# Kernel tuning notes

Hardware: AMD Instinct MI355X
Metric: run time of the kernel (lower is better)

## Reference

```python
import jax, jax.numpy as jnp
import numpy as np

D_MODEL = 1024
NUM_HEADS = 16
D_K = D_MODEL // NUM_HEADS
ROPE_THETA = 10000.0


def setup_inputs() -> dict:
    key = jax.random.key(0)
    kx, kq, kk, kv, ko = jax.random.split(key, 5)
    B, S = 2, 2048
    sigma = np.sqrt(2.0) / np.sqrt(D_MODEL + D_MODEL)
    x = jax.random.normal(kx, (B, S, D_MODEL), dtype=jnp.float32)
    Wq = jax.random.normal(kq, (D_MODEL, D_MODEL), dtype=jnp.float32) * sigma
    Wk = jax.random.normal(kk, (D_MODEL, D_MODEL), dtype=jnp.float32) * sigma
    Wv = jax.random.normal(kv, (D_MODEL, D_MODEL), dtype=jnp.float32) * sigma
    Wo = jax.random.normal(ko, (D_MODEL, D_MODEL), dtype=jnp.float32) * sigma
    return {"x": x, "Wq": Wq, "Wk": Wk, "Wv": Wv, "Wo": Wo}


def _rope(t, positions):
    # t: [B, H, S, D_K], positions: [S]
    half = jnp.arange(0, D_K, 2, dtype=jnp.float32)          # [D_K/2]
    freqs = 1.0 / (ROPE_THETA ** (half / D_K))               # [D_K/2]
    angles = positions[:, None].astype(jnp.float32) * freqs  # [S, D_K/2]
    cos = jnp.cos(angles)
    sin = jnp.sin(angles)
    t_even = t[..., 0::2]
    t_odd = t[..., 1::2]
    even_rot = t_even * cos - t_odd * sin
    odd_rot = t_even * sin + t_odd * cos
    # interleave back to [..., D_K]
    return jnp.stack([even_rot, odd_rot], axis=-1).reshape(t.shape)


def reference(x, Wq, Wk, Wv, Wo):
    B, S, _ = x.shape
    # weight layout is [d_out, d_in]: y = x @ W.T
    def proj(W):
        y = jnp.einsum('bsd,ed->bse', x, W)
        return y.reshape(B, S, NUM_HEADS, D_K).transpose(0, 2, 1, 3)  # [B,H,S,Dk]
    Q, K, V = proj(Wq), proj(Wk), proj(Wv)
    positions = jnp.arange(S)
    Q = _rope(Q, positions)
    K = _rope(K, positions)
    scale = 1.0 / jnp.sqrt(jnp.asarray(D_K, dtype=x.dtype))
    scores = jnp.einsum('bhqd,bhkd->bhqk', Q, K) * scale  # [B,H,S,S]
    causal = jnp.tril(jnp.ones((S, S), dtype=bool))
    scores = jnp.where(causal, scores, -jnp.inf)
    probs = jax.nn.softmax(scores, axis=-1)
    out = jnp.einsum('bhqk,bhkd->bhqd', probs, V)          # [B,H,S,Dk]
    out = out.transpose(0, 2, 1, 3).reshape(B, S, D_MODEL)
    return jnp.einsum('bsd,ed->bse', out, Wo)
```

## Files before the change

kernel.cpp:

```cpp
#include <hip/hip_runtime.h>
#include <hip/hip_bf16.h>
#include <math.h>

#define S_LEN   2048
#define BATCH   2
#define DMODEL  1024
#define NHEADS  16
#define DKH     64
#define MROWS   (BATCH * S_LEN)

typedef __attribute__((ext_vector_type(8))) __bf16 bf16x8;
typedef __attribute__((ext_vector_type(4))) float f32x4;
typedef __attribute__((ext_vector_type(8))) unsigned short u16x8;

__device__ __forceinline__ float bfu2f(unsigned short u) {
    union { unsigned int i; float f; } v;
    v.i = ((unsigned int)u) << 16;
    return v.f;
}

__device__ __forceinline__ unsigned short f2bfu(float f) {
    union { __bf16 h; unsigned short u; } v;
    v.h = (__bf16)f;
    return v.u;
}

#define LGKM0() __builtin_amdgcn_s_waitcnt(0xc07f)

#define SROW 40

__global__ __launch_bounds__(256) void gemm_qkv(
    const float* __restrict__ X,
    const float* __restrict__ W0, const float* __restrict__ W1, const float* __restrict__ W2,
    unsigned short* __restrict__ Yq, unsigned short* __restrict__ Yk, unsigned short* __restrict__ Yv)
{
    __shared__ __align__(16) unsigned char pool[36864];
    unsigned short* As = (unsigned short*)pool;
    unsigned short* Bs = As + 128 * SROW;

    const int tid  = threadIdx.x;
    const int wave = tid >> 6;
    const int lane = tid & 63;
    const int c    = lane & 15;
    const int quad = lane >> 4;

    const int m0 = blockIdx.y * 128;
    const int n0 = blockIdx.x * 128;
    const int w_idx = n0 >> 10;
    const int e0    = n0 & 1023;
    const float* W = (w_idx == 0) ? W0 : (w_idx == 1) ? W1 : W2;

    const int mhalf = (wave & 1) * 64;
    const int nhalf = (wave >> 1) * 64;

    f32x4 acc[4][4];
#pragma unroll
    for (int i = 0; i < 4; i++)
#pragma unroll
        for (int j = 0; j < 4; j++) acc[i][j] = (f32x4){0.f, 0.f, 0.f, 0.f};

    const int lrow = tid >> 3;
    const int lkq  = tid & 7;

    float4 rA[4], rB[4];
#pragma unroll
    for (int i = 0; i < 4; i++) {
        rA[i] = *(const float4*)(X + (size_t)(m0 + i * 32 + lrow) * DMODEL + lkq * 4);
        rB[i] = *(const float4*)(W + (size_t)(e0 + i * 32 + lrow) * DMODEL + lkq * 4);
    }

    for (int k0 = 0; k0 < DMODEL; k0 += 32) {
        __syncthreads();
#pragma unroll
        for (int i = 0; i < 4; i++) {
            ushort4 h;
            h.x = f2bfu(rA[i].x); h.y = f2bfu(rA[i].y); h.z = f2bfu(rA[i].z); h.w = f2bfu(rA[i].w);
            *(ushort4*)(&As[(i * 32 + lrow) * SROW + lkq * 4]) = h;
        }
#pragma unroll
        for (int i = 0; i < 4; i++) {
            ushort4 h;
            h.x = f2bfu(rB[i].x); h.y = f2bfu(rB[i].y); h.z = f2bfu(rB[i].z); h.w = f2bfu(rB[i].w);
            *(ushort4*)(&Bs[(i * 32 + lrow) * SROW + lkq * 4]) = h;
        }
        __syncthreads();

        if (k0 + 32 < DMODEL) {
#pragma unroll
            for (int i = 0; i < 4; i++) {
                rA[i] = *(const float4*)(X + (size_t)(m0 + i * 32 + lrow) * DMODEL + k0 + 32 + lkq * 4);
                rB[i] = *(const float4*)(W + (size_t)(e0 + i * 32 + lrow) * DMODEL + k0 + 32 + lkq * 4);
            }
        }

        bf16x8 af[4], bfr[4];
#pragma unroll
        for (int mt = 0; mt < 4; mt++)
            af[mt] = *(const bf16x8*)(&As[(mhalf + mt * 16 + c) * SROW + quad * 8]);
#pragma unroll
        for (int nt = 0; nt < 4; nt++)
            bfr[nt] = *(const bf16x8*)(&Bs[(nhalf + nt * 16 + c) * SROW + quad * 8]);
#pragma unroll
        for (int mt = 0; mt < 4; mt++)
#pragma unroll
            for (int nt = 0; nt < 4; nt++)
                acc[mt][nt] = __builtin_amdgcn_mfma_f32_16x16x32_bf16(af[mt], bfr[nt], acc[mt][nt], 0, 0, 0);
    }

    __syncthreads();

    const int h = (e0 + nhalf) >> 6;
    if (w_idx < 2) {
        unsigned short* Yqk = (w_idx == 0) ? Yq : Yk;
        float* EPf = (float*)pool + wave * 16 * 68;
        const int row = lane >> 2;
        const int cg  = lane & 3;
#pragma unroll
        for (int mt = 0; mt < 4; mt++) {
            LGKM0();
#pragma unroll
            for (int nt = 0; nt < 4; nt++)
#pragma unroll
                for (int r = 0; r < 4; r++)
                    EPf[(quad * 4 + r) * 68 + nt * 16 + c] = acc[mt][nt][r];
            LGKM0();
            float fl[16];
#pragma unroll
            for (int j = 0; j < 4; j++) {
                float4 v = *(const float4*)(&EPf[row * 68 + cg * 16 + j * 4]);
                fl[j * 4 + 0] = v.x; fl[j * 4 + 1] = v.y;
                fl[j * 4 + 2] = v.z; fl[j * 4 + 3] = v.w;
            }
            int m = m0 + mhalf + mt * 16 + row;
            int s = m & (S_LEN - 1);
            int b = m >> 11;
            u16x8 o0, o1;
#pragma unroll
            for (int pi = 0; pi < 8; pi++) {
                int p = cg * 8 + pi;
                float freq  = exp2f(-(float)p * 0.41524101186092034f);
                float angle = (float)s * freq;
                float sn, cs;
                __sincosf(angle, &sn, &cs);
                float ev = fl[2 * pi], ov = fl[2 * pi + 1];
                float re = ev * cs - ov * sn;
                float ro = ev * sn + ov * cs;
                if (pi < 4) { o0[2 * pi] = f2bfu(re); o0[2 * pi + 1] = f2bfu(ro); }
                else        { o1[2 * (pi - 4)] = f2bfu(re); o1[2 * (pi - 4) + 1] = f2bfu(ro); }
            }
            unsigned short* dst = Yqk + (((size_t)(b * NHEADS + h)) * S_LEN + s) * DKH + cg * 16;
            *(u16x8*)(dst)     = o0;
            *(u16x8*)(dst + 8) = o1;
        }
    } else {
        unsigned short* EPb = (unsigned short*)pool + wave * 64 * 72;
        LGKM0();
#pragma unroll
        for (int nt = 0; nt < 4; nt++)
#pragma unroll
            for (int mt = 0; mt < 4; mt++)
#pragma unroll
                for (int r = 0; r < 4; r++)
                    EPb[(nt * 16 + c) * 72 + mt * 16 + quad * 4 + r] = f2bfu(acc[mt][nt][r]);
        LGKM0();
        int mbase = m0 + mhalf;
        int s0 = mbase & (S_LEN - 1);
        int b  = mbase >> 11;
        unsigned short* dst = Yv + (((size_t)(b * NHEADS + h)) * DKH + lane) * S_LEN + s0;
#pragma unroll
        for (int j = 0; j < 8; j++)
            *(u16x8*)(dst + j * 8) = *(const u16x8*)(&EPb[lane * 72 + j * 8]);
    }
}

__global__ __launch_bounds__(256) void gemm_wo(
    const unsigned short* __restrict__ X,
    const float* __restrict__ W,
    float* __restrict__ Yf)
{
    __shared__ __align__(16) unsigned char pool[17408];
    unsigned short* As = (unsigned short*)pool;
    unsigned short* Bs = As + 64 * SROW;

    const int tid  = threadIdx.x;
    const int wave = tid >> 6;
    const int lane = tid & 63;
    const int c    = lane & 15;
    const int quad = lane >> 4;

    const int m0 = blockIdx.y * 64;
    const int n0 = blockIdx.x * 128;

    const int mhalf = (wave & 1) * 32;
    const int nhalf = (wave >> 1) * 64;

    f32x4 acc[2][4];
#pragma unroll
    for (int i = 0; i < 2; i++)
#pragma unroll
        for (int j = 0; j < 4; j++) acc[i][j] = (f32x4){0.f, 0.f, 0.f, 0.f};

    const int lrow = tid >> 3;
    const int lkq  = tid & 7;

    ushort4 rA[2];
    float4  rB[4];
#pragma unroll
    for (int i = 0; i < 2; i++)
        rA[i] = *(const ushort4*)(X + (size_t)(m0 + i * 32 + lrow) * DMODEL + lkq * 4);
#pragma unroll
    for (int i = 0; i < 4; i++)
        rB[i] = *(const float4*)(W + (size_t)(n0 + i * 32 + lrow) * DMODEL + lkq * 4);

    for (int k0 = 0; k0 < DMODEL; k0 += 32) {
        __syncthreads();
#pragma unroll
        for (int i = 0; i < 2; i++)
            *(ushort4*)(&As[(i * 32 + lrow) * SROW + lkq * 4]) = rA[i];
#pragma unroll
        for (int i = 0; i < 4; i++) {
            ushort4 h;
            h.x = f2bfu(rB[i].x); h.y = f2bfu(rB[i].y); h.z = f2bfu(rB[i].z); h.w = f2bfu(rB[i].w);
            *(ushort4*)(&Bs[(i * 32 + lrow) * SROW + lkq * 4]) = h;
        }
        __syncthreads();

        if (k0 + 32 < DMODEL) {
#pragma unroll
            for (int i = 0; i < 2; i++)
                rA[i] = *(const ushort4*)(X + (size_t)(m0 + i * 32 + lrow) * DMODEL + k0 + 32 + lkq * 4);
#pragma unroll
            for (int i = 0; i < 4; i++)
                rB[i] = *(const float4*)(W + (size_t)(n0 + i * 32 + lrow) * DMODEL + k0 + 32 + lkq * 4);
        }

        bf16x8 af[2], bfr[4];
#pragma unroll
        for (int mt = 0; mt < 2; mt++)
            af[mt] = *(const bf16x8*)(&As[(mhalf + mt * 16 + c) * SROW + quad * 8]);
#pragma unroll
        for (int nt = 0; nt < 4; nt++)
            bfr[nt] = *(const bf16x8*)(&Bs[(nhalf + nt * 16 + c) * SROW + quad * 8]);
#pragma unroll
        for (int mt = 0; mt < 2; mt++)
#pragma unroll
            for (int nt = 0; nt < 4; nt++)
                acc[mt][nt] = __builtin_amdgcn_mfma_f32_16x16x32_bf16(af[mt], bfr[nt], acc[mt][nt], 0, 0, 0);
    }

    __syncthreads();

    float* EPf = (float*)pool + wave * 16 * 68;
    const int row = lane >> 2;
    const int cg  = lane & 3;
#pragma unroll
    for (int mt = 0; mt < 2; mt++) {
        LGKM0();
#pragma unroll
        for (int nt = 0; nt < 4; nt++)
#pragma unroll
            for (int r = 0; r < 4; r++)
                EPf[(quad * 4 + r) * 68 + nt * 16 + c] = acc[mt][nt][r];
        LGKM0();
        int m = m0 + mhalf + mt * 16 + row;
        float* dst = Yf + (size_t)m * DMODEL + n0 + nhalf + cg * 16;
#pragma unroll
        for (int j = 0; j < 4; j++)
            *(float4*)(dst + j * 4) = *(const float4*)(&EPf[row * 68 + cg * 16 + j * 4]);
    }
}

__global__ __launch_bounds__(256, 4) void attn_mfma(
    const unsigned short* __restrict__ Q,
    const unsigned short* __restrict__ K,
    const unsigned short* __restrict__ Vt,
    unsigned short* __restrict__ A)
{
    __shared__ unsigned short Ks[32 * 72];
    __shared__ unsigned short Vs[64 * 40];
    __shared__ unsigned short Plds[4][16 * 40];

    const int tid  = threadIdx.x;
    const int wave = tid >> 6;
    const int lane = tid & 63;
    const int c    = lane & 15;
    const int quad = lane >> 4;

    const int bh = blockIdx.x;
    const int b  = bh >> 4;
    const int h  = bh & 15;
    const int qb = (int)(gridDim.y - 1) - (int)blockIdx.y;
    const int q0b = qb * 64;
    const int q0 = q0b + wave * 16;

    const unsigned short* Qb = Q  + (size_t)bh * S_LEN * DKH;
    const unsigned short* Kb = K  + (size_t)bh * S_LEN * DKH;
    const unsigned short* Vb = Vt + (size_t)bh * DKH * S_LEN;

    bf16x8 qf0 = *(const bf16x8*)(Qb + (q0 + c) * DKH + quad * 8);
    bf16x8 qf1 = *(const bf16x8*)(Qb + (q0 + c) * DKH + 32 + quad * 8);

    f32x4 o0 = {0.f,0.f,0.f,0.f}, o1 = o0, o2 = o0, o3 = o0;
    float l[4] = {0.f, 0.f, 0.f, 0.f};

    unsigned short* Pw = &Plds[wave][0];

    const int my_nkb   = (q0 + 16 + 31) >> 5;
    const int nkb_blk  = (q0b + 64 + 31) >> 5;
    const int kb_full  = (q0 >= 31) ? (((q0 - 31) >> 5) + 1) : 0;

    const int krow  = tid >> 3;
    const int kcol8 = (tid & 7) * 8;
    const int vrow  = tid >> 2;
    const int vcol8 = (tid & 3) * 8;

    uint4 gK = *(const uint4*)(Kb + (size_t)krow * DKH + kcol8);
    uint4 gV = *(const uint4*)(Vb + (size_t)vrow * S_LEN + vcol8);

    for (int kb = 0; kb < nkb_blk; kb++) {
        const int k0 = kb * 32;
        __syncthreads();
        *(uint4*)(&Ks[krow * 72 + kcol8]) = gK;
        *(uint4*)(&Vs[vrow * 40 + vcol8]) = gV;
        __syncthreads();
        if (kb + 1 < nkb_blk) {
            gK = *(const uint4*)(Kb + (size_t)(k0 + 32 + krow) * DKH + kcol8);
            gV = *(const uint4*)(Vb + (size_t)vrow * S_LEN + k0 + 32 + vcol8);
        }
        if (kb < my_nkb) {
            bf16x8 k00 = *(const bf16x8*)(&Ks[c * 72 + quad * 8]);
            bf16x8 k01 = *(const bf16x8*)(&Ks[c * 72 + 32 + quad * 8]);
            bf16x8 k10 = *(const bf16x8*)(&Ks[(16 + c) * 72 + quad * 8]);
            bf16x8 k11 = *(const bf16x8*)(&Ks[(16 + c) * 72 + 32 + quad * 8]);
            f32x4 s0 = {0.f,0.f,0.f,0.f}, s1 = {0.f,0.f,0.f,0.f};
            s0 = __builtin_amdgcn_mfma_f32_16x16x32_bf16(qf0, k00, s0, 0, 0, 0);
            s0 = __builtin_amdgcn_mfma_f32_16x16x32_bf16(qf1, k01, s0, 0, 0, 0);
            s1 = __builtin_amdgcn_mfma_f32_16x16x32_bf16(qf0, k10, s1, 0, 0, 0);
            s1 = __builtin_amdgcn_mfma_f32_16x16x32_bf16(qf1, k11, s1, 0, 0, 0);

            if (kb < kb_full) {
#pragma unroll
                for (int r = 0; r < 4; r++) {
                    float e0 = __expf(s0[r] * 0.125f);
                    float e1 = __expf(s1[r] * 0.125f);
                    unsigned short pb0 = f2bfu(e0);
                    unsigned short pb1 = f2bfu(e1);
                    Pw[(quad * 4 + r) * 40 + c]      = pb0;
                    Pw[(quad * 4 + r) * 40 + 16 + c] = pb1;
                    l[r] += bfu2f(pb0) + bfu2f(pb1);
                }
            } else {
#pragma unroll
                for (int r = 0; r < 4; r++) {
                    int qrow = q0 + quad * 4 + r;
                    float e0 = (k0 + c      <= qrow) ? __expf(s0[r] * 0.125f) : 0.0f;
                    float e1 = (k0 + 16 + c <= qrow) ? __expf(s1[r] * 0.125f) : 0.0f;
                    unsigned short pb0 = f2bfu(e0);
                    unsigned short pb1 = f2bfu(e1);
                    Pw[(quad * 4 + r) * 40 + c]      = pb0;
                    Pw[(quad * 4 + r) * 40 + 16 + c] = pb1;
                    l[r] += bfu2f(pb0) + bfu2f(pb1);
                }
            }
            LGKM0();

            bf16x8 pf = *(const bf16x8*)(Pw + c * 40 + quad * 8);

            bf16x8 vf0 = *(const bf16x8*)(&Vs[(0 * 16 + c) * 40 + quad * 8]);
            bf16x8 vf1 = *(const bf16x8*)(&Vs[(1 * 16 + c) * 40 + quad * 8]);
            bf16x8 vf2 = *(const bf16x8*)(&Vs[(2 * 16 + c) * 40 + quad * 8]);
            bf16x8 vf3 = *(const bf16x8*)(&Vs[(3 * 16 + c) * 40 + quad * 8]);
            o0 = __builtin_amdgcn_mfma_f32_16x16x32_bf16(pf, vf0, o0, 0, 0, 0);
            o1 = __builtin_amdgcn_mfma_f32_16x16x32_bf16(pf, vf1, o1, 0, 0, 0);
            o2 = __builtin_amdgcn_mfma_f32_16x16x32_bf16(pf, vf2, o2, 0, 0, 0);
            o3 = __builtin_amdgcn_mfma_f32_16x16x32_bf16(pf, vf3, o3, 0, 0, 0);
        }
    }

#pragma unroll
    for (int m = 1; m < 16; m <<= 1) {
#pragma unroll
        for (int r = 0; r < 4; r++) l[r] += __shfl_xor(l[r], m, 64);
    }

#pragma unroll
    for (int r = 0; r < 4; r++) {
        float inv = 1.0f / l[r];
        int s = q0 + quad * 4 + r;
        unsigned short* Ap = A + ((size_t)b * S_LEN + s) * DMODEL + h * DKH;
        Ap[0 * 16 + c] = f2bfu(o0[r] * inv);
        Ap[1 * 16 + c] = f2bfu(o1[r] * inv);
        Ap[2 * 16 + c] = f2bfu(o2[r] * inv);
        Ap[3 * 16 + c] = f2bfu(o3[r] * inv);
    }
}

extern "C" void kernel_launch(void* const* d_in, const int* in_sizes, int n_in,
                              void* d_out, int out_size, void* d_ws, size_t ws_size,
                              hipStream_t stream) {
    const float* x  = (const float*)d_in[0];
    const float* Wq = (const float*)d_in[1];
    const float* Wk = (const float*)d_in[2];
    const float* Wv = (const float*)d_in[3];
    const float* Wo = (const float*)d_in[4];
    float* out = (float*)d_out;

    unsigned short* Qw = (unsigned short*)d_ws;
    unsigned short* Kw = Qw + (size_t)MROWS * DMODEL;
    unsigned short* Vw = Kw + (size_t)MROWS * DMODEL;
    unsigned short* Aw = Vw + (size_t)MROWS * DMODEL;

    gemm_qkv<<<dim3(3 * DMODEL / 128, MROWS / 128), 256, 0, stream>>>(
        x, Wq, Wk, Wv, Qw, Kw, Vw);

    attn_mfma<<<dim3(NHEADS * BATCH, S_LEN / 64), 256, 0, stream>>>(Qw, Kw, Vw, Aw);

    gemm_wo<<<dim3(DMODEL / 128, MROWS / 64), 256, 0, stream>>>(Aw, Wo, out);
}
```

Baseline: 202.1 us.

## Enlarge attention KV tile to 64 and drop register prefetch in QKV GEMM

The attention kernel now stages 64-key K/V tiles per iteration instead of 32. This halves the number of barrier-separated iterations and issues more MFMAs per LDS round trip. The per-wave early skip of fully masked tiles is removed, so causal masking is handled entirely in the masked-tile branch. The QKV projection GEMM drops its register double-buffer and loads the global fp32 tile inside the loop just before converting it to LDS. That shortens register live ranges but gives up the overlap of global loads with MFMA work.

New measurement: 196.5 us. 1.03x faster.

```diff
diff --git a/kernel.cpp b/kernel.cpp
--- a/kernel.cpp
+++ b/kernel.cpp
@@ -62,36 +62,25 @@
     const int lrow = tid >> 3;
     const int lkq  = tid & 7;
 
-    float4 rA[4], rB[4];
-#pragma unroll
-    for (int i = 0; i < 4; i++) {
-        rA[i] = *(const float4*)(X + (size_t)(m0 + i * 32 + lrow) * DMODEL + lkq * 4);
-        rB[i] = *(const float4*)(W + (size_t)(e0 + i * 32 + lrow) * DMODEL + lkq * 4);
-    }
-
     for (int k0 = 0; k0 < DMODEL; k0 += 32) {
         __syncthreads();
 #pragma unroll
         for (int i = 0; i < 4; i++) {
+            int row = i * 32 + lrow;
+            float4 v = *(const float4*)(X + (size_t)(m0 + row) * DMODEL + k0 + lkq * 4);
             ushort4 h;
-            h.x = f2bfu(rA[i].x); h.y = f2bfu(rA[i].y); h.z = f2bfu(rA[i].z); h.w = f2bfu(rA[i].w);
-            *(ushort4*)(&As[(i * 32 + lrow) * SROW + lkq * 4]) = h;
+            h.x = f2bfu(v.x); h.y = f2bfu(v.y); h.z = f2bfu(v.z); h.w = f2bfu(v.w);
+            *(ushort4*)(&As[row * SROW + lkq * 4]) = h;
         }
 #pragma unroll
         for (int i = 0; i < 4; i++) {
+            int row = i * 32 + lrow;
+            float4 v = *(const float4*)(W + (size_t)(e0 + row) * DMODEL + k0 + lkq * 4);
             ushort4 h;
-            h.x = f2bfu(rB[i].x); h.y = f2bfu(rB[i].y); h.z = f2bfu(rB[i].z); h.w = f2bfu(rB[i].w);
-            *(ushort4*)(&Bs[(i * 32 + lrow) * SROW + lkq * 4]) = h;
-        }
-        __syncthreads();
-
-        if (k0 + 32 < DMODEL) {
-#pragma unroll
-            for (int i = 0; i < 4; i++) {
-                rA[i] = *(const float4*)(X + (size_t)(m0 + i * 32 + lrow) * DMODEL + k0 + 32 + lkq * 4);
-                rB[i] = *(const float4*)(W + (size_t)(e0 + i * 32 + lrow) * DMODEL + k0 + 32 + lkq * 4);
-            }
-        }
+            h.x = f2bfu(v.x); h.y = f2bfu(v.y); h.z = f2bfu(v.z); h.w = f2bfu(v.w);
+            *(ushort4*)(&Bs[row * SROW + lkq * 4]) = h;
+        }
+        __syncthreads();
 
         bf16x8 af[4], bfr[4];
 #pragma unroll
@@ -276,9 +265,9 @@
     const unsigned short* __restrict__ Vt,
     unsigned short* __restrict__ A)
 {
-    __shared__ unsigned short Ks[32 * 72];
-    __shared__ unsigned short Vs[64 * 40];
-    __shared__ unsigned short Plds[4][16 * 40];
+    __shared__ unsigned short Ks[64 * 72];
+    __shared__ unsigned short Vs[64 * 72];
+    __shared__ unsigned short Plds[4][16 * 72];
 
     const int tid  = threadIdx.x;
     const int wave = tid >> 6;
@@ -290,8 +279,7 @@
     const int b  = bh >> 4;
     const int h  = bh & 15;
     const int qb = (int)(gridDim.y - 1) - (int)blockIdx.y;
-    const int q0b = qb * 64;
-    const int q0 = q0b + wave * 16;
+    const int q0 = qb * 64 + wave * 16;
 
     const unsigned short* Qb = Q  + (size_t)bh * S_LEN * DKH;
     const unsigned short* Kb = K  + (size_t)bh * S_LEN * DKH;
@@ -300,80 +288,82 @@
     bf16x8 qf0 = *(const bf16x8*)(Qb + (q0 + c) * DKH + quad * 8);
     bf16x8 qf1 = *(const bf16x8*)(Qb + (q0 + c) * DKH + 32 + quad * 8);
 
-    f32x4 o0 = {0.f,0.f,0.f,0.f}, o1 = o0, o2 = o0, o3 = o0;
+    f32x4 o[4];
+#pragma unroll
+    for (int dt = 0; dt < 4; dt++) o[dt] = (f32x4){0.f,0.f,0.f,0.f};
     float l[4] = {0.f, 0.f, 0.f, 0.f};
 
     unsigned short* Pw = &Plds[wave][0];
 
-    const int my_nkb   = (q0 + 16 + 31) >> 5;
-    const int nkb_blk  = (q0b + 64 + 31) >> 5;
-    const int kb_full  = (q0 >= 31) ? (((q0 - 31) >> 5) + 1) : 0;
-
-    const int krow  = tid >> 3;
-    const int kcol8 = (tid & 7) * 8;
-    const int vrow  = tid >> 2;
-    const int vcol8 = (tid & 3) * 8;
-
-    uint4 gK = *(const uint4*)(Kb + (size_t)krow * DKH + kcol8);
-    uint4 gV = *(const uint4*)(Vb + (size_t)vrow * S_LEN + vcol8);
-
-    for (int kb = 0; kb < nkb_blk; kb++) {
-        const int k0 = kb * 32;
-        __syncthreads();
-        *(uint4*)(&Ks[krow * 72 + kcol8]) = gK;
-        *(uint4*)(&Vs[vrow * 40 + vcol8]) = gV;
-        __syncthreads();
-        if (kb + 1 < nkb_blk) {
-            gK = *(const uint4*)(Kb + (size_t)(k0 + 32 + krow) * DKH + kcol8);
-            gV = *(const uint4*)(Vb + (size_t)vrow * S_LEN + k0 + 32 + vcol8);
-        }
-        if (kb < my_nkb) {
-            bf16x8 k00 = *(const bf16x8*)(&Ks[c * 72 + quad * 8]);
-            bf16x8 k01 = *(const bf16x8*)(&Ks[c * 72 + 32 + quad * 8]);
-            bf16x8 k10 = *(const bf16x8*)(&Ks[(16 + c) * 72 + quad * 8]);
-            bf16x8 k11 = *(const bf16x8*)(&Ks[(16 + c) * 72 + 32 + quad * 8]);
-            f32x4 s0 = {0.f,0.f,0.f,0.f}, s1 = {0.f,0.f,0.f,0.f};
-            s0 = __builtin_amdgcn_mfma_f32_16x16x32_bf16(qf0, k00, s0, 0, 0, 0);
-            s0 = __builtin_amdgcn_mfma_f32_16x16x32_bf16(qf1, k01, s0, 0, 0, 0);
-            s1 = __builtin_amdgcn_mfma_f32_16x16x32_bf16(qf0, k10, s1, 0, 0, 0);
-            s1 = __builtin_amdgcn_mfma_f32_16x16x32_bf16(qf1, k11, s1, 0, 0, 0);
-
-            if (kb < kb_full) {
+    const int nkb     = qb + 1;
+    const int kb_full = (q0 >= 63) ? (((q0 - 63) >> 6) + 1) : 0;
+
+    const int srow = tid >> 2;
+    const int scol = (tid & 3) * 16;
+
+    uint4 gK0 = *(const uint4*)(Kb + (size_t)srow * DKH + scol);
+    uint4 gK1 = *(const uint4*)(Kb + (size_t)srow * DKH + scol + 8);
+    uint4 gV0 = *(const uint4*)(Vb + (size_t)srow * S_LEN + scol);
+    uint4 gV1 = *(const uint4*)(Vb + (size_t)srow * S_LEN + scol + 8);
+
+    for (int kb = 0; kb < nkb; kb++) {
+        const int k0 = kb * 64;
+        __syncthreads();
+        *(uint4*)(&Ks[srow * 72 + scol])     = gK0;
+        *(uint4*)(&Ks[srow * 72 + scol + 8]) = gK1;
+        *(uint4*)(&Vs[srow * 72 + scol])     = gV0;
+        *(uint4*)(&Vs[srow * 72 + scol + 8]) = gV1;
+        __syncthreads();
+        if (kb + 1 < nkb) {
+            gK0 = *(const uint4*)(Kb + (size_t)(k0 + 64 + srow) * DKH + scol);
+            gK1 = *(const uint4*)(Kb + (size_t)(k0 + 64 + srow) * DKH + scol + 8);
+            gV0 = *(const uint4*)(Vb + (size_t)srow * S_LEN + k0 + 64 + scol);
+            gV1 = *(const uint4*)(Vb + (size_t)srow * S_LEN + k0 + 64 + scol + 8);
+        }
+
+        f32x4 s[4];
+#pragma unroll
+        for (int t = 0; t < 4; t++) {
+            bf16x8 kA = *(const bf16x8*)(&Ks[(t * 16 + c) * 72 + quad * 8]);
+            bf16x8 kB = *(const bf16x8*)(&Ks[(t * 16 + c) * 72 + 32 + quad * 8]);
+            f32x4 z = {0.f,0.f,0.f,0.f};
+            z = __builtin_amdgcn_mfma_f32_16x16x32_bf16(qf0, kA, z, 0, 0, 0);
+            z = __builtin_amdgcn_mfma_f32_16x16x32_bf16(qf1, kB, z, 0, 0, 0);
+            s[t] = z;
+        }
+
+        if (kb < kb_full) {
+#pragma unroll
+            for (int t = 0; t < 4; t++)
 #pragma unroll
                 for (int r = 0; r < 4; r++) {
-                    float e0 = __expf(s0[r] * 0.125f);
-                    float e1 = __expf(s1[r] * 0.125f);
-                    unsigned short pb0 = f2bfu(e0);
-                    unsigned short pb1 = f2bfu(e1);
-                    Pw[(quad * 4 + r) * 40 + c]      = pb0;
-                    Pw[(quad * 4 + r) * 40 + 16 + c] = pb1;
-                    l[r] += bfu2f(pb0) + bfu2f(pb1);
+                    unsigned short pb = f2bfu(__expf(s[t][r] * 0.125f));
+                    Pw[(quad * 4 + r) * 72 + t * 16 + c] = pb;
+                    l[r] += bfu2f(pb);
                 }
-            } else {
+        } else {
+#pragma unroll
+            for (int t = 0; t < 4; t++)
 #pragma unroll
                 for (int r = 0; r < 4; r++) {
                     int qrow = q0 + quad * 4 + r;
-                    float e0 = (k0 + c      <= qrow) ? __expf(s0[r] * 0.125f) : 0.0f;
-                    float e1 = (k0 + 16 + c <= qrow) ? __expf(s1[r] * 0.125f) : 0.0f;
-                    unsigned short pb0 = f2bfu(e0);
-                    unsigned short pb1 = f2bfu(e1);
-                    Pw[(quad * 4 + r) * 40 + c]      = pb0;
-                    Pw[(quad * 4 + r) * 40 + 16 + c] = pb1;
-                    l[r] += bfu2f(pb0) + bfu2f(pb1);
+                    float e = (k0 + t * 16 + c <= qrow) ? __expf(s[t][r] * 0.125f) : 0.0f;
+                    unsigned short pb = f2bfu(e);
+                    Pw[(quad * 4 + r) * 72 + t * 16 + c] = pb;
+                    l[r] += bfu2f(pb);
                 }
-            }
-            LGKM0();
-
-            bf16x8 pf = *(const bf16x8*)(Pw + c * 40 + quad * 8);
-
-            bf16x8 vf0 = *(const bf16x8*)(&Vs[(0 * 16 + c) * 40 + quad * 8]);
-            bf16x8 vf1 = *(const bf16x8*)(&Vs[(1 * 16 + c) * 40 + quad * 8]);
-            bf16x8 vf2 = *(const bf16x8*)(&Vs[(2 * 16 + c) * 40 + quad * 8]);
-            bf16x8 vf3 = *(const bf16x8*)(&Vs[(3 * 16 + c) * 40 + quad * 8]);
-            o0 = __builtin_amdgcn_mfma_f32_16x16x32_bf16(pf, vf0, o0, 0, 0, 0);
-            o1 = __builtin_amdgcn_mfma_f32_16x16x32_bf16(pf, vf1, o1, 0, 0, 0);
-            o2 = __builtin_amdgcn_mfma_f32_16x16x32_bf16(pf, vf2, o2, 0, 0, 0);
-            o3 = __builtin_amdgcn_mfma_f32_16x16x32_bf16(pf, vf3, o3, 0, 0, 0);
+        }
+        LGKM0();
+
+        bf16x8 pf0 = *(const bf16x8*)(Pw + c * 72 + quad * 8);
+        bf16x8 pf1 = *(const bf16x8*)(Pw + c * 72 + 32 + quad * 8);
+
+#pragma unroll
+        for (int dt = 0; dt < 4; dt++) {
+            bf16x8 vA = *(const bf16x8*)(&Vs[(dt * 16 + c) * 72 + quad * 8]);
+            bf16x8 vB = *(const bf16x8*)(&Vs[(dt * 16 + c) * 72 + 32 + quad * 8]);
+            o[dt] = __builtin_amdgcn_mfma_f32_16x16x32_bf16(pf0, vA, o[dt], 0, 0, 0);
+            o[dt] = __builtin_amdgcn_mfma_f32_16x16x32_bf16(pf1, vB, o[dt], 0, 0, 0);
         }
     }
 
@@ -388,10 +378,10 @@
         float inv = 1.0f / l[r];
         int s = q0 + quad * 4 + r;
         unsigned short* Ap = A + ((size_t)b * S_LEN + s) * DMODEL + h * DKH;
-        Ap[0 * 16 + c] = f2bfu(o0[r] * inv);
-        Ap[1 * 16 + c] = f2bfu(o1[r] * inv);
-        Ap[2 * 16 + c] = f2bfu(o2[r] * inv);
-        Ap[3 * 16 + c] = f2bfu(o3[r] * inv);
+        Ap[0 * 16 + c] = f2bfu(o[0][r] * inv);
+        Ap[1 * 16 + c] = f2bfu(o[1][r] * inv);
+        Ap[2 * 16 + c] = f2bfu(o[2][r] * inv);
+        Ap[3 * 16 + c] = f2bfu(o[3][r] * inv);
     }
 }
 
```

## Pre-convert QKV weights to bf16 and widen Wo GEMM K-tile

Applied to the files above, without the earlier changes.

Adds a separate kernel that converts Wq/Wk/Wv to bf16 once per call into workspace. gemm_qkv then loads bf16 weights directly, which halves weight traffic and removes the per-tile conversion across the 32 M-blocks. Its register prefetch double-buffering is dropped, so global loads are no longer overlapped with MFMA. gemm_wo moves to 64-wide K tiles with 16-byte loads, and the weight buffer's workspace slot is reused for the attention output.

Result: faster. 193.9 us (-4.0%).

```diff
diff --git a/kernel.cpp b/kernel.cpp
--- a/kernel.cpp
+++ b/kernel.cpp
@@ -29,9 +29,23 @@
 
 #define SROW 40
 
+__global__ __launch_bounds__(256) void cvt_w(
+    const float* __restrict__ W0, const float* __restrict__ W1, const float* __restrict__ W2,
+    unsigned short* __restrict__ Wb)
+{
+    const float* W = (blockIdx.y == 0) ? W0 : (blockIdx.y == 1) ? W1 : W2;
+    size_t idx = ((size_t)blockIdx.x * 256 + threadIdx.x) * 8;
+    float4 a = *(const float4*)(W + idx);
+    float4 b = *(const float4*)(W + idx + 4);
+    u16x8 h;
+    h[0] = f2bfu(a.x); h[1] = f2bfu(a.y); h[2] = f2bfu(a.z); h[3] = f2bfu(a.w);
+    h[4] = f2bfu(b.x); h[5] = f2bfu(b.y); h[6] = f2bfu(b.z); h[7] = f2bfu(b.w);
+    *(u16x8*)(Wb + (size_t)blockIdx.y * (DMODEL * DMODEL) + idx) = h;
+}
+
 __global__ __launch_bounds__(256) void gemm_qkv(
     const float* __restrict__ X,
-    const float* __restrict__ W0, const float* __restrict__ W1, const float* __restrict__ W2,
+    const unsigned short* __restrict__ Wb,
     unsigned short* __restrict__ Yq, unsigned short* __restrict__ Yk, unsigned short* __restrict__ Yv)
 {
     __shared__ __align__(16) unsigned char pool[36864];
@@ -48,7 +62,7 @@
     const int n0 = blockIdx.x * 128;
     const int w_idx = n0 >> 10;
     const int e0    = n0 & 1023;
-    const float* W = (w_idx == 0) ? W0 : (w_idx == 1) ? W1 : W2;
+    const unsigned short* Wsrc = Wb + (size_t)w_idx * (DMODEL * DMODEL);
 
     const int mhalf = (wave & 1) * 64;
     const int nhalf = (wave >> 1) * 64;
@@ -61,37 +75,26 @@
 
     const int lrow = tid >> 3;
     const int lkq  = tid & 7;
-
-    float4 rA[4], rB[4];
-#pragma unroll
-    for (int i = 0; i < 4; i++) {
-        rA[i] = *(const float4*)(X + (size_t)(m0 + i * 32 + lrow) * DMODEL + lkq * 4);
-        rB[i] = *(const float4*)(W + (size_t)(e0 + i * 32 + lrow) * DMODEL + lkq * 4);
-    }
+    const int brow = tid >> 2;
+    const int bchk = (tid & 3) * 8;
 
     for (int k0 = 0; k0 < DMODEL; k0 += 32) {
         __syncthreads();
 #pragma unroll
         for (int i = 0; i < 4; i++) {
+            int row = i * 32 + lrow;
+            float4 v = *(const float4*)(X + (size_t)(m0 + row) * DMODEL + k0 + lkq * 4);
             ushort4 h;
-            h.x = f2bfu(rA[i].x); h.y = f2bfu(rA[i].y); h.z = f2bfu(rA[i].z); h.w = f2bfu(rA[i].w);
-            *(ushort4*)(&As[(i * 32 + lrow) * SROW + lkq * 4]) = h;
-        }
-#pragma unroll
-        for (int i = 0; i < 4; i++) {
-            ushort4 h;
-            h.x = f2bfu(rB[i].x); h.y = f2bfu(rB[i].y); h.z = f2bfu(rB[i].z); h.w = f2bfu(rB[i].w);
-            *(ushort4*)(&Bs[(i * 32 + lrow) * SROW + lkq * 4]) = h;
-        }
-        __syncthreads();
-
-        if (k0 + 32 < DMODEL) {
-#pragma unroll
-            for (int i = 0; i < 4; i++) {
-                rA[i] = *(const float4*)(X + (size_t)(m0 + i * 32 + lrow) * DMODEL + k0 + 32 + lkq * 4);
-                rB[i] = *(const float4*)(W + (size_t)(e0 + i * 32 + lrow) * DMODEL + k0 + 32 + lkq * 4);
-            }
-        }
+            h.x = f2bfu(v.x); h.y = f2bfu(v.y); h.z = f2bfu(v.z); h.w = f2bfu(v.w);
+            *(ushort4*)(&As[row * SROW + lkq * 4]) = h;
+        }
+#pragma unroll
+        for (int i = 0; i < 2; i++) {
+            int row = i * 64 + brow;
+            *(u16x8*)(&Bs[row * SROW + bchk]) =
+                *(const u16x8*)(Wsrc + (size_t)(e0 + row) * DMODEL + k0 + bchk);
+        }
+        __syncthreads();
 
         bf16x8 af[4], bfr[4];
 #pragma unroll
@@ -178,9 +181,9 @@
     const float* __restrict__ W,
     float* __restrict__ Yf)
 {
-    __shared__ __align__(16) unsigned char pool[17408];
+    __shared__ __align__(16) unsigned char pool[27648];
     unsigned short* As = (unsigned short*)pool;
-    unsigned short* Bs = As + 64 * SROW;
+    unsigned short* Bs = As + 64 * 72;
 
     const int tid  = threadIdx.x;
     const int wave = tid >> 6;
@@ -200,52 +203,45 @@
 #pragma unroll
         for (int j = 0; j < 4; j++) acc[i][j] = (f32x4){0.f, 0.f, 0.f, 0.f};
 
-    const int lrow = tid >> 3;
-    const int lkq  = tid & 7;
-
-    ushort4 rA[2];
-    float4  rB[4];
-#pragma unroll
-    for (int i = 0; i < 2; i++)
-        rA[i] = *(const ushort4*)(X + (size_t)(m0 + i * 32 + lrow) * DMODEL + lkq * 4);
-#pragma unroll
-    for (int i = 0; i < 4; i++)
-        rB[i] = *(const float4*)(W + (size_t)(n0 + i * 32 + lrow) * DMODEL + lkq * 4);
-
-    for (int k0 = 0; k0 < DMODEL; k0 += 32) {
-        __syncthreads();
-#pragma unroll
-        for (int i = 0; i < 2; i++)
-            *(ushort4*)(&As[(i * 32 + lrow) * SROW + lkq * 4]) = rA[i];
+    const int srow = tid >> 3;
+    const int scol = (tid & 7) * 8;
+
+    for (int k0 = 0; k0 < DMODEL; k0 += 64) {
+        __syncthreads();
+#pragma unroll
+        for (int i = 0; i < 2; i++) {
+            int row = i * 32 + srow;
+            *(u16x8*)(&As[row * 72 + scol]) =
+                *(const u16x8*)(X + (size_t)(m0 + row) * DMODEL + k0 + scol);
+        }
 #pragma unroll
         for (int i = 0; i < 4; i++) {
-            ushort4 h;
-            h.x = f2bfu(rB[i].x); h.y = f2bfu(rB[i].y); h.z = f2bfu(rB[i].z); h.w = f2bfu(rB[i].w);
-            *(ushort4*)(&Bs[(i * 32 + lrow) * SROW + lkq * 4]) = h;
-        }
-        __syncthreads();
-
-        if (k0 + 32 < DMODEL) {
-#pragma unroll
-            for (int i = 0; i < 2; i++)
-                rA[i] = *(const ushort4*)(X + (size_t)(m0 + i * 32 + lrow) * DMODEL + k0 + 32 + lkq * 4);
-#pragma unroll
-            for (int i = 0; i < 4; i++)
-                rB[i] = *(const float4*)(W + (size_t)(n0 + i * 32 + lrow) * DMODEL + k0 + 32 + lkq * 4);
-        }
-
-        bf16x8 af[2], bfr[4];
-#pragma unroll
-        for (int mt = 0; mt < 2; mt++)
-            af[mt] = *(const bf16x8*)(&As[(mhalf + mt * 16 + c) * SROW + quad * 8]);
-#pragma unroll
-        for (int nt = 0; nt < 4; nt++)
-            bfr[nt] = *(const bf16x8*)(&Bs[(nhalf + nt * 16 + c) * SROW + quad * 8]);
-#pragma unroll
-        for (int mt = 0; mt < 2; mt++)
+            int row = i * 32 + srow;
+            const float* p = W + (size_t)(n0 + row) * DMODEL + k0 + scol;
+            float4 va = *(const float4*)(p);
+            float4 vb = *(const float4*)(p + 4);
+            u16x8 h;
+            h[0] = f2bfu(va.x); h[1] = f2bfu(va.y); h[2] = f2bfu(va.z); h[3] = f2bfu(va.w);
+            h[4] = f2bfu(vb.x); h[5] = f2bfu(vb.y); h[6] = f2bfu(vb.z); h[7] = f2bfu(vb.w);
+            *(u16x8*)(&Bs[row * 72 + scol]) = h;
+        }
+        __syncthreads();
+
+#pragma unroll
+        for (int half = 0; half < 2; half++) {
+            bf16x8 af[2], bfr[4];
+#pragma unroll
+            for (int mt = 0; mt < 2; mt++)
+                af[mt] = *(const bf16x8*)(&As[(mhalf + mt * 16 + c) * 72 + half * 32 + quad * 8]);
 #pragma unroll
             for (int nt = 0; nt < 4; nt++)
-                acc[mt][nt] = __builtin_amdgcn_mfma_f32_16x16x32_bf16(af[mt], bfr[nt], acc[mt][nt], 0, 0, 0);
+                bfr[nt] = *(const bf16x8*)(&Bs[(nhalf + nt * 16 + c) * 72 + half * 32 + quad * 8]);
+#pragma unroll
+            for (int mt = 0; mt < 2; mt++)
+#pragma unroll
+                for (int nt = 0; nt < 4; nt++)
+                    acc[mt][nt] = __builtin_amdgcn_mfma_f32_16x16x32_bf16(af[mt], bfr[nt], acc[mt][nt], 0, 0, 0);
+        }
     }
 
     __syncthreads();
@@ -408,10 +404,13 @@
     unsigned short* Qw = (unsigned short*)d_ws;
     unsigned short* Kw = Qw + (size_t)MROWS * DMODEL;
     unsigned short* Vw = Kw + (size_t)MROWS * DMODEL;
-    unsigned short* Aw = Vw + (size_t)MROWS * DMODEL;
+    unsigned short* Wb = Vw + (size_t)MROWS * DMODEL;
+    unsigned short* Aw = Wb;
+
+    cvt_w<<<dim3(DMODEL * DMODEL / (256 * 8), 3), 256, 0, stream>>>(Wq, Wk, Wv, Wb);
 
     gemm_qkv<<<dim3(3 * DMODEL / 128, MROWS / 128), 256, 0, stream>>>(
-        x, Wq, Wk, Wv, Qw, Kw, Vw);
+        x, Wb, Qw, Kw, Vw);
 
     attn_mfma<<<dim3(NHEADS * BATCH, S_LEN / 64), 256, 0, stream>>>(Qw, Kw, Vw, Aw);
 
```
